# Kernel tuning notes

Measured on AMD Instinct MI355X. Metric: run time of the kernel, lower is better.

Reference implementation:

```python
import jax, jax.numpy as jnp
import numpy as np

R = 32
LORA_ALPHA = 64
SCALING = LORA_ALPHA / R  # 2.0
TOPK = 2
NOISE_EPS = 0.01


def setup_inputs() -> dict:
    key = jax.random.key(0)
    ks = jax.random.split(key, 7)
    B, S, D, OUT, E = 4, 2048, 4096, 4096, 8
    x = jax.random.normal(ks[0], (B, S, D), dtype=jnp.float32)
    eof_index = jax.random.randint(ks[1], (B,), 0, S)
    noise = jax.random.normal(ks[2], (B, E), dtype=jnp.float32)
    # learned params (random instead of the zero-init in reset_parameters so the
    # output is non-trivial); Linear weight layout is [out_features, in_features]
    A_w = jax.random.normal(ks[3], (R, D), dtype=jnp.float32) * (1.0 / np.sqrt(D))
    B_w = jax.random.normal(ks[4], (E, OUT, R), dtype=jnp.float32) * (1.0 / np.sqrt(R))
    route_w = jax.random.normal(ks[5], (E, D), dtype=jnp.float32) * (1.0 / np.sqrt(D))
    noise_w = jax.random.normal(ks[6], (E, D), dtype=jnp.float32) * (1.0 / np.sqrt(D))
    return {"x": x, "eof_index": eof_index, "noise": noise,
            "A_w": A_w, "B_w": B_w, "route_w": route_w, "noise_w": noise_w}


def reference(x, eof_index, noise, A_w, B_w, route_w, noise_w):
    B = x.shape[0]
    rows = jnp.arange(B)
    # routing input: token at eof_index for each batch row -> [B, D]
    routing_input = x[rows, eof_index]
    # noisy top-k gating (training path: noisy_gating and is_train are True)
    clean_logits = routing_input @ route_w.T                       # [B, E]
    noise_stddev = jax.nn.softplus(routing_input @ noise_w.T) + NOISE_EPS
    logits = clean_logits + noise * noise_stddev                   # [B, E]
    # torch code takes topk+1 then slices to topk; equivalent to top_k(topk)
    top_vals, top_idx = jax.lax.top_k(logits, TOPK)                # [B, K]
    top_gates = jax.nn.softmax(top_vals.astype(jnp.float32), axis=-1).astype(x.dtype)
    gates = jnp.zeros_like(logits).at[rows[:, None], top_idx].set(top_gates)  # [B, E]
    # shared low-rank projection
    shared = jnp.einsum('bsd,rd->bsr', x, A_w)                     # [B, S, r]
    # sum_i gate_i * (shared @ B_i^T), fused as one contraction
    lora_output = jnp.einsum('bsr,eor,be->bso', shared, B_w, gates)  # [B, S, out]
    return lora_output * SCALING
```

## Files before the change

### kernel.cpp

```cpp
#include <hip/hip_runtime.h>
#include <stdint.h>
#include <math.h>

#define B_ 4
#define S_ 2048
#define D_ 4096
#define O_ 4096
#define E_ 8
#define R_ 32
#define SCALING 2.0f
#define NOISE_EPS 0.01f

typedef unsigned short u16;
typedef short s16x8 __attribute__((ext_vector_type(8)));
typedef float f32x4 __attribute__((ext_vector_type(4)));

__device__ __forceinline__ float b2f(u16 u) {
  union { unsigned int i; float f; } v; v.i = ((unsigned int)u) << 16; return v.f;
}
__device__ __forceinline__ u16 f2b(float f) {
  union { unsigned int i; float f; } v; v.f = f;
  unsigned int i = v.i;
  return (u16)((i + 0x7FFFu + ((i >> 16) & 1u)) >> 16);
}
__device__ __forceinline__ void split2(float f, u16* h, u16* l) {
  u16 hi = f2b(f);
  *h = hi;
  *l = f2b(f - b2f(hi));
}

__device__ __forceinline__ float ld(const void* p, size_t i, int bf) {
  return bf ? b2f(((const u16*)p)[i]) : ((const float*)p)[i];
}

__global__ void k_detect(const unsigned int* __restrict__ xw, int* __restrict__ flag) {
  __shared__ int cnt;
  if (threadIdx.x == 0) cnt = 0;
  __syncthreads();
  unsigned int w = xw[threadIdx.x];
  unsigned int e = (w >> 7) & 0xFFu;
  if (e >= 90u && e <= 140u) atomicAdd(&cnt, 1);
  __syncthreads();
  if (threadIdx.x == 0) *flag = (cnt > 48) ? 1 : 0;
}

__global__ __launch_bounds__(256) void k_logits(
    const void* __restrict__ x, const int* __restrict__ eof,
    const void* __restrict__ route_w, const void* __restrict__ noise_w,
    const int* __restrict__ flag, float* __restrict__ wsf) {
  int bf = *flag;
  int be = blockIdx.x;
  int b = be >> 3, e = be & 7;
  size_t xoff = ((size_t)b * S_ + (size_t)eof[b]) * D_;
  size_t woff = (size_t)e * D_;
  float ac = 0.f, an = 0.f;
  for (int d = threadIdx.x; d < D_; d += 256) {
    float xv = ld(x, xoff + d, bf);
    ac += xv * ld(route_w, woff + d, bf);
    an += xv * ld(noise_w, woff + d, bf);
  }
  __shared__ float rc[256], rn[256];
  rc[threadIdx.x] = ac; rn[threadIdx.x] = an;
  __syncthreads();
  for (int s = 128; s > 0; s >>= 1) {
    if (threadIdx.x < (unsigned)s) {
      rc[threadIdx.x] += rc[threadIdx.x + s];
      rn[threadIdx.x] += rn[threadIdx.x + s];
    }
    __syncthreads();
  }
  if (threadIdx.x == 0) { wsf[16 + be] = rc[0]; wsf[48 + be] = rn[0]; }
}

__global__ void k_gates(const void* __restrict__ noise, const int* __restrict__ flag,
                        float* __restrict__ wsf) {
  int bf = *flag;
  int b = threadIdx.x;
  if (b >= B_) return;
  float lg[E_];
  for (int e = 0; e < E_; e++) {
    float c = wsf[16 + b * 8 + e];
    float n = wsf[48 + b * 8 + e];
    float sp = (n > 20.f) ? n : log1pf(expf(n));
    lg[e] = c + ld(noise, b * 8 + e, bf) * (sp + NOISE_EPS);
  }
  int i1 = 0; float v1 = lg[0];
  for (int e = 1; e < E_; e++) if (lg[e] > v1) { v1 = lg[e]; i1 = e; }
  int i2 = -1; float v2 = -3.0e38f;
  for (int e = 0; e < E_; e++) if (e != i1 && lg[e] > v2) { v2 = lg[e]; i2 = e; }
  float t = expf(v2 - v1);
  float g1 = 1.f / (1.f + t);
  float g2 = t / (1.f + t);
  for (int e = 0; e < E_; e++) wsf[80 + b * 8 + e] = 0.f;
  wsf[80 + b * 8 + i1] = g1;
  wsf[80 + b * 8 + i2] = g2;
}

__global__ __launch_bounds__(256) void k_prep(
    const void* __restrict__ Bw, const float* __restrict__ Aw,
    const int* __restrict__ flag, const float* __restrict__ gates,
    u16* __restrict__ Wph, u16* __restrict__ Wpl,
    u16* __restrict__ Aph, u16* __restrict__ Apl) {
  int bf = *flag;
  int blk = blockIdx.x;
  if (blk < 512) {
    int idx = blk * 256 + threadIdx.x;
    int b = idx >> 15;
    int u = idx & 32767;
    int o = u >> 3, rq = u & 7;
    float g[E_];
#pragma unroll
    for (int e = 0; e < E_; e++) g[e] = gates[b * 8 + e];
    f32x4 acc = {0.f, 0.f, 0.f, 0.f};
    if (bf) {
#pragma unroll
      for (int e = 0; e < E_; e++) {
        ushort4 v = ((const ushort4*)Bw)[(size_t)e * 32768 + u];
        acc[0] += g[e] * b2f(v.x);
        acc[1] += g[e] * b2f(v.y);
        acc[2] += g[e] * b2f(v.z);
        acc[3] += g[e] * b2f(v.w);
      }
    } else {
#pragma unroll
      for (int e = 0; e < E_; e++) {
        f32x4 v = ((const f32x4*)Bw)[(size_t)e * 32768 + u];
        acc += g[e] * v;
      }
    }
    acc *= SCALING;
    ushort4 h, l;
    split2(acc[0], &h.x, &l.x); split2(acc[1], &h.y, &l.y);
    split2(acc[2], &h.z, &l.z); split2(acc[3], &h.w, &l.w);
    int ot = o >> 4;
    int lane = ((rq >> 1) * 16) + (o & 15);
    size_t base = (((size_t)b * 256 + ot) * 64 + lane) * 8 + (rq & 1) * 4;
    *(ushort4*)(Wph + base) = h;
    *(ushort4*)(Wpl + base) = l;
  } else {
    if (bf) return;
    int flat = (blk - 512) * 256 + threadIdx.x;
    int k32idx = flat >> 7;
    int rem = flat & 127;
    int hf = rem >> 6;
    int lane = rem & 63;
    int r = hf * 16 + (lane & 15);
    int d = k32idx * 32 + (lane >> 4) * 8;
    const float* src = Aw + (size_t)r * D_ + d;
    f32x4 v0 = *(const f32x4*)src;
    f32x4 v1 = *(const f32x4*)(src + 4);
    ushort4 h0, l0, h1, l1;
    split2(v0[0], &h0.x, &l0.x); split2(v0[1], &h0.y, &l0.y);
    split2(v0[2], &h0.z, &l0.z); split2(v0[3], &h0.w, &l0.w);
    split2(v1[0], &h1.x, &l1.x); split2(v1[1], &h1.y, &l1.y);
    split2(v1[2], &h1.z, &l1.z); split2(v1[3], &h1.w, &l1.w);
    *(ushort4*)(Aph + (size_t)flat * 8)     = h0;
    *(ushort4*)(Aph + (size_t)flat * 8 + 4) = h1;
    *(ushort4*)(Apl + (size_t)flat * 8)     = l0;
    *(ushort4*)(Apl + (size_t)flat * 8 + 4) = l1;
  }
}

#define OCH 512
__global__ __launch_bounds__(256) void k_mega(
    const void* __restrict__ xv, const void* __restrict__ Awv,
    const u16* __restrict__ Aph, const u16* __restrict__ Apl,
    const u16* __restrict__ Wph, const u16* __restrict__ Wpl,
    const int* __restrict__ flag, void* __restrict__ out) {
  __shared__ union SM {
    struct { u16 xh[4096]; u16 xl[4096]; float red[4][512]; } p1;
    float C[16][516];
  } sm;
  __shared__ u16 shAh[512], shAl[512];
  int bf = *flag;
  int t = threadIdx.x;
  int lane = t & 63;
  int wave = t >> 6;
  int m = lane & 15, kg = lane >> 4;
  int row0 = blockIdx.x * 16;
  int b = row0 >> 11;

  f32x4 acc0 = {0.f, 0.f, 0.f, 0.f};
  f32x4 acc1 = {0.f, 0.f, 0.f, 0.f};
  if (bf) {
    int kbase = wave * 1024 + kg * 8;
    const u16* xp = (const u16*)xv + (size_t)(row0 + m) * D_ + kbase;
    const u16* a0 = (const u16*)Awv + (size_t)m * D_ + kbase;
    const u16* a1 = (const u16*)Awv + (size_t)(m + 16) * D_ + kbase;
#pragma unroll 4
    for (int k0 = 0; k0 < 1024; k0 += 32) {
      s16x8 a  = *(const s16x8*)(xp + k0);
      s16x8 b0 = *(const s16x8*)(a0 + k0);
      s16x8 b1 = *(const s16x8*)(a1 + k0);
      acc0 = __builtin_amdgcn_mfma_f32_16x16x32_bf16(a, b0, acc0, 0, 0, 0);
      acc1 = __builtin_amdgcn_mfma_f32_16x16x32_bf16(a, b1, acc1, 0, 0, 0);
    }
  } else {
    int srow = t >> 4;
    int sq = t & 15;
    const float* xrow = (const float*)xv + (size_t)(row0 + srow) * D_;
    for (int kc = 0; kc < D_; kc += 256) {
      __syncthreads();
#pragma unroll
      for (int q = 0; q < 4; q++) {
        int colf = (sq + q * 16) * 4;
        f32x4 v = *(const f32x4*)(xrow + kc + colf);
        ushort4 h, l;
        split2(v[0], &h.x, &l.x); split2(v[1], &h.y, &l.y);
        split2(v[2], &h.z, &l.z); split2(v[3], &h.w, &l.w);
        int swz = (srow * 512 + colf * 2) ^ ((srow & 7) << 4);
        *(ushort4*)((char*)sm.p1.xh + swz) = h;
        *(ushort4*)((char*)sm.p1.xl + swz) = l;
      }
      __syncthreads();
#pragma unroll
      for (int p = 0; p < 2; p++) {
        int k32 = (wave * 2 + p) * 32;
        int boff = (m * 512 + (k32 + kg * 8) * 2) ^ ((m & 7) << 4);
        s16x8 ah = *(const s16x8*)((const char*)sm.p1.xh + boff);
        s16x8 al = *(const s16x8*)((const char*)sm.p1.xl + boff);
        size_t k32idx = (size_t)(kc >> 5) + wave * 2 + p;
        const u16* ph = Aph + (k32idx * 2) * 512;
        const u16* pl = Apl + (k32idx * 2) * 512;
        s16x8 bh0 = *(const s16x8*)(ph + (size_t)lane * 8);
        s16x8 bl0 = *(const s16x8*)(pl + (size_t)lane * 8);
        s16x8 bh1 = *(const s16x8*)(ph + 512 + (size_t)lane * 8);
        s16x8 bl1 = *(const s16x8*)(pl + 512 + (size_t)lane * 8);
        acc0 = __builtin_amdgcn_mfma_f32_16x16x32_bf16(ah, bh0, acc0, 0, 0, 0);
        acc0 = __builtin_amdgcn_mfma_f32_16x16x32_bf16(ah, bl0, acc0, 0, 0, 0);
        acc0 = __builtin_amdgcn_mfma_f32_16x16x32_bf16(al, bh0, acc0, 0, 0, 0);
        acc1 = __builtin_amdgcn_mfma_f32_16x16x32_bf16(ah, bh1, acc1, 0, 0, 0);
        acc1 = __builtin_amdgcn_mfma_f32_16x16x32_bf16(ah, bl1, acc1, 0, 0, 0);
        acc1 = __builtin_amdgcn_mfma_f32_16x16x32_bf16(al, bh1, acc1, 0, 0, 0);
      }
    }
  }
  __syncthreads();
  int crow = (lane >> 4) * 4, ccol = lane & 15;
#pragma unroll
  for (int j = 0; j < 4; j++) {
    sm.p1.red[wave][(crow + j) * 32 + ccol]      = acc0[j];
    sm.p1.red[wave][(crow + j) * 32 + ccol + 16] = acc1[j];
  }
  __syncthreads();
#pragma unroll
  for (int q = 0; q < 2; q++) {
    int e = t + q * 256;
    float s = sm.p1.red[0][e] + sm.p1.red[1][e] + sm.p1.red[2][e] + sm.p1.red[3][e];
    u16 h, l;
    split2(s, &h, &l);
    int row = e >> 5, r = e & 31;
    int dst = ((r >> 3) * 16 + row) * 8 + (r & 7);
    shAh[dst] = h;
    shAl[dst] = l;
  }
  __syncthreads();

  s16x8 Ah = *(const s16x8*)(shAh + (size_t)lane * 8);
  s16x8 Al = *(const s16x8*)(shAl + (size_t)lane * 8);
  const u16* whB = Wph + (size_t)b * 131072;
  const u16* wlB = Wpl + (size_t)b * 131072;
  for (int oc = 0; oc < O_; oc += OCH) {
    __syncthreads();
#pragma unroll
    for (int i = 0; i < 8; i++) {
      int otc = wave * 8 + i;
      size_t otg = (size_t)((oc >> 4) + otc);
      s16x8 Bh = *(const s16x8*)(whB + otg * 512 + (size_t)lane * 8);
      s16x8 Bl = *(const s16x8*)(wlB + otg * 512 + (size_t)lane * 8);
      f32x4 acc = {0.f, 0.f, 0.f, 0.f};
      acc = __builtin_amdgcn_mfma_f32_16x16x32_bf16(Ah, Bh, acc, 0, 0, 0);
      acc = __builtin_amdgcn_mfma_f32_16x16x32_bf16(Ah, Bl, acc, 0, 0, 0);
      acc = __builtin_amdgcn_mfma_f32_16x16x32_bf16(Al, Bh, acc, 0, 0, 0);
      int ocol = otc * 16 + m;
#pragma unroll
      for (int j = 0; j < 4; j++) sm.C[crow + j][ocol] = acc[j];
    }
    __syncthreads();
#pragma unroll
    for (int it = 0; it < 8; it++) {
      int row = it * 2 + (t >> 7);
      int col = (t & 127) * 4;
      f32x4 v = *(const f32x4*)&sm.C[row][col];
      size_t off = (size_t)(row0 + row) * O_ + oc + col;
      if (bf) {
        ushort4 o4;
        o4.x = f2b(v[0]); o4.y = f2b(v[1]); o4.z = f2b(v[2]); o4.w = f2b(v[3]);
        *(ushort4*)((u16*)out + off) = o4;
      } else {
        *(f32x4*)((float*)out + off) = v;
      }
    }
  }
}

extern "C" void kernel_launch(void* const* d_in, const int* in_sizes, int n_in,
                              void* d_out, int out_size, void* d_ws, size_t ws_size,
                              hipStream_t stream) {
  const void* x       = d_in[0];
  const int*  eof     = (const int*)d_in[1];
  const void* noise   = d_in[2];
  const void* Aw      = d_in[3];
  const void* Bw      = d_in[4];
  const void* route_w = d_in[5];
  const void* noise_w = d_in[6];
  float* wsf = (float*)d_ws;
  int* flag = (int*)wsf;
  float* gates = wsf + 80;
  u16* Wph  = (u16*)(wsf + 112);
  u16* Wpl  = Wph + (size_t)B_ * O_ * R_;
  u16* Aph  = Wpl + (size_t)B_ * O_ * R_;
  u16* Apl  = Aph + (size_t)R_ * D_;

  k_detect<<<1, 64, 0, stream>>>((const unsigned int*)x, flag);
  k_logits<<<B_ * E_, 256, 0, stream>>>(x, eof, route_w, noise_w, flag, wsf);
  k_gates<<<1, 64, 0, stream>>>(noise, flag, wsf);
  k_prep<<<512 + 64, 256, 0, stream>>>(Bw, (const float*)Aw, flag, gates,
                                       Wph, Wpl, Aph, Apl);
  k_mega<<<(B_ * S_) / 16, 256, 0, stream>>>(x, Aw, Aph, Apl, Wph, Wpl,
                                             flag, d_out);
}
```

Measured before the change: 303.6 us.

## Split fused kernel into K-split projection and output-split expansion kernels

Removes the separate detect and gates kernels: each kernel now detects the input dtype with a wave ballot, and the gate computation is folded into k_prep. The single fused kernel is split in two. k_sharedP splits the D reduction four ways and writes partial rank-32 projections to a workspace buffer. k_outP sums those partials and computes a quarter of the output columns per block. This raises the block count from 512 to 2048 per stage for better CU occupancy and cuts launches, at the cost of an extra global round trip for the partials and redundant gate math per thread.

Result: faster. 285.8 us (median of 2 runs) (-5.8%).

```diff
diff --git a/kernel.cpp b/kernel.cpp
--- a/kernel.cpp
+++ b/kernel.cpp
@@ -33,22 +33,18 @@
   return bf ? b2f(((const u16*)p)[i]) : ((const float*)p)[i];
 }
 
-__global__ void k_detect(const unsigned int* __restrict__ xw, int* __restrict__ flag) {
-  __shared__ int cnt;
-  if (threadIdx.x == 0) cnt = 0;
-  __syncthreads();
-  unsigned int w = xw[threadIdx.x];
+__device__ __forceinline__ int detect_bf(const unsigned int* __restrict__ xw) {
+  unsigned int w = xw[threadIdx.x & 63];
   unsigned int e = (w >> 7) & 0xFFu;
-  if (e >= 90u && e <= 140u) atomicAdd(&cnt, 1);
-  __syncthreads();
-  if (threadIdx.x == 0) *flag = (cnt > 48) ? 1 : 0;
+  unsigned long long mask = __ballot((e >= 90u) && (e <= 140u));
+  return (__popcll(mask) > 48) ? 1 : 0;
 }
 
 __global__ __launch_bounds__(256) void k_logits(
     const void* __restrict__ x, const int* __restrict__ eof,
     const void* __restrict__ route_w, const void* __restrict__ noise_w,
-    const int* __restrict__ flag, float* __restrict__ wsf) {
-  int bf = *flag;
+    float* __restrict__ wsf) {
+  int bf = detect_bf((const unsigned int*)x);
   int be = blockIdx.x;
   int b = be >> 3, e = be & 7;
   size_t xoff = ((size_t)b * S_ + (size_t)eof[b]) * D_;
@@ -72,45 +68,40 @@
   if (threadIdx.x == 0) { wsf[16 + be] = rc[0]; wsf[48 + be] = rn[0]; }
 }
 
-__global__ void k_gates(const void* __restrict__ noise, const int* __restrict__ flag,
-                        float* __restrict__ wsf) {
-  int bf = *flag;
-  int b = threadIdx.x;
-  if (b >= B_) return;
-  float lg[E_];
-  for (int e = 0; e < E_; e++) {
-    float c = wsf[16 + b * 8 + e];
-    float n = wsf[48 + b * 8 + e];
-    float sp = (n > 20.f) ? n : log1pf(expf(n));
-    lg[e] = c + ld(noise, b * 8 + e, bf) * (sp + NOISE_EPS);
-  }
-  int i1 = 0; float v1 = lg[0];
-  for (int e = 1; e < E_; e++) if (lg[e] > v1) { v1 = lg[e]; i1 = e; }
-  int i2 = -1; float v2 = -3.0e38f;
-  for (int e = 0; e < E_; e++) if (e != i1 && lg[e] > v2) { v2 = lg[e]; i2 = e; }
-  float t = expf(v2 - v1);
-  float g1 = 1.f / (1.f + t);
-  float g2 = t / (1.f + t);
-  for (int e = 0; e < E_; e++) wsf[80 + b * 8 + e] = 0.f;
-  wsf[80 + b * 8 + i1] = g1;
-  wsf[80 + b * 8 + i2] = g2;
-}
-
 __global__ __launch_bounds__(256) void k_prep(
     const void* __restrict__ Bw, const float* __restrict__ Aw,
-    const int* __restrict__ flag, const float* __restrict__ gates,
+    const void* __restrict__ noise, const void* __restrict__ x,
+    const float* __restrict__ wsf,
     u16* __restrict__ Wph, u16* __restrict__ Wpl,
     u16* __restrict__ Aph, u16* __restrict__ Apl) {
-  int bf = *flag;
+  int bf = detect_bf((const unsigned int*)x);
   int blk = blockIdx.x;
   if (blk < 512) {
     int idx = blk * 256 + threadIdx.x;
     int b = idx >> 15;
+    float lg[E_];
+#pragma unroll
+    for (int e = 0; e < E_; e++) {
+      float c = wsf[16 + b * 8 + e];
+      float n = wsf[48 + b * 8 + e];
+      float sp = (n > 20.f) ? n : log1pf(expf(n));
+      lg[e] = c + ld(noise, b * 8 + e, bf) * (sp + NOISE_EPS);
+    }
+    int i1 = 0; float v1 = lg[0];
+#pragma unroll
+    for (int e = 1; e < E_; e++) if (lg[e] > v1) { v1 = lg[e]; i1 = e; }
+    int i2 = -1; float v2 = -3.0e38f;
+#pragma unroll
+    for (int e = 0; e < E_; e++) if (e != i1 && lg[e] > v2) { v2 = lg[e]; i2 = e; }
+    float tt = expf(v2 - v1);
+    float g1 = 1.f / (1.f + tt);
+    float g2 = tt / (1.f + tt);
+    float g[E_];
+#pragma unroll
+    for (int e = 0; e < E_; e++) g[e] = 0.f;
+    g[i1] = g1; g[i2] = g2;
     int u = idx & 32767;
     int o = u >> 3, rq = u & 7;
-    float g[E_];
-#pragma unroll
-    for (int e = 0; e < E_; e++) g[e] = gates[b * 8 + e];
     f32x4 acc = {0.f, 0.f, 0.f, 0.f};
     if (bf) {
 #pragma unroll
@@ -161,34 +152,31 @@
   }
 }
 
-#define OCH 512
-__global__ __launch_bounds__(256) void k_mega(
+__global__ __launch_bounds__(256) void k_sharedP(
     const void* __restrict__ xv, const void* __restrict__ Awv,
     const u16* __restrict__ Aph, const u16* __restrict__ Apl,
-    const u16* __restrict__ Wph, const u16* __restrict__ Wpl,
-    const int* __restrict__ flag, void* __restrict__ out) {
-  __shared__ union SM {
-    struct { u16 xh[4096]; u16 xl[4096]; float red[4][512]; } p1;
-    float C[16][516];
+    float* __restrict__ pbuf) {
+  __shared__ union {
+    struct { u16 xh[4096]; u16 xl[4096]; } s;
+    float red4[4][512];
   } sm;
-  __shared__ u16 shAh[512], shAl[512];
-  int bf = *flag;
+  int bf = detect_bf((const unsigned int*)xv);
   int t = threadIdx.x;
   int lane = t & 63;
   int wave = t >> 6;
   int m = lane & 15, kg = lane >> 4;
-  int row0 = blockIdx.x * 16;
-  int b = row0 >> 11;
-
+  int rowgrp = blockIdx.x >> 2;
+  int dq = blockIdx.x & 3;
+  int row0 = rowgrp * 16;
   f32x4 acc0 = {0.f, 0.f, 0.f, 0.f};
   f32x4 acc1 = {0.f, 0.f, 0.f, 0.f};
   if (bf) {
-    int kbase = wave * 1024 + kg * 8;
+    int kbase = dq * 1024 + wave * 256 + kg * 8;
     const u16* xp = (const u16*)xv + (size_t)(row0 + m) * D_ + kbase;
     const u16* a0 = (const u16*)Awv + (size_t)m * D_ + kbase;
     const u16* a1 = (const u16*)Awv + (size_t)(m + 16) * D_ + kbase;
-#pragma unroll 4
-    for (int k0 = 0; k0 < 1024; k0 += 32) {
+#pragma unroll
+    for (int k0 = 0; k0 < 256; k0 += 32) {
       s16x8 a  = *(const s16x8*)(xp + k0);
       s16x8 b0 = *(const s16x8*)(a0 + k0);
       s16x8 b1 = *(const s16x8*)(a1 + k0);
@@ -198,30 +186,30 @@
   } else {
     int srow = t >> 4;
     int sq = t & 15;
-    const float* xrow = (const float*)xv + (size_t)(row0 + srow) * D_;
-    for (int kc = 0; kc < D_; kc += 256) {
+    const float* xrow = (const float*)xv + (size_t)(row0 + srow) * D_ + dq * 1024;
+    for (int c = 0; c < 4; c++) {
       __syncthreads();
 #pragma unroll
       for (int q = 0; q < 4; q++) {
         int colf = (sq + q * 16) * 4;
-        f32x4 v = *(const f32x4*)(xrow + kc + colf);
+        f32x4 v = *(const f32x4*)(xrow + c * 256 + colf);
         ushort4 h, l;
         split2(v[0], &h.x, &l.x); split2(v[1], &h.y, &l.y);
         split2(v[2], &h.z, &l.z); split2(v[3], &h.w, &l.w);
         int swz = (srow * 512 + colf * 2) ^ ((srow & 7) << 4);
-        *(ushort4*)((char*)sm.p1.xh + swz) = h;
-        *(ushort4*)((char*)sm.p1.xl + swz) = l;
+        *(ushort4*)((char*)sm.s.xh + swz) = h;
+        *(ushort4*)((char*)sm.s.xl + swz) = l;
       }
       __syncthreads();
 #pragma unroll
-      for (int p = 0; p < 2; p++) {
-        int k32 = (wave * 2 + p) * 32;
+      for (int p2 = 0; p2 < 2; p2++) {
+        int k32 = (wave * 2 + p2) * 32;
         int boff = (m * 512 + (k32 + kg * 8) * 2) ^ ((m & 7) << 4);
-        s16x8 ah = *(const s16x8*)((const char*)sm.p1.xh + boff);
-        s16x8 al = *(const s16x8*)((const char*)sm.p1.xl + boff);
-        size_t k32idx = (size_t)(kc >> 5) + wave * 2 + p;
-        const u16* ph = Aph + (k32idx * 2) * 512;
-        const u16* pl = Apl + (k32idx * 2) * 512;
+        s16x8 ah = *(const s16x8*)((const char*)sm.s.xh + boff);
+        s16x8 al = *(const s16x8*)((const char*)sm.s.xl + boff);
+        int k32idx = dq * 32 + c * 8 + wave * 2 + p2;
+        const u16* ph = Aph + (size_t)k32idx * 1024;
+        const u16* pl = Apl + (size_t)k32idx * 1024;
         s16x8 bh0 = *(const s16x8*)(ph + (size_t)lane * 8);
         s16x8 bl0 = *(const s16x8*)(pl + (size_t)lane * 8);
         s16x8 bh1 = *(const s16x8*)(ph + 512 + (size_t)lane * 8);
@@ -239,33 +227,66 @@
   int crow = (lane >> 4) * 4, ccol = lane & 15;
 #pragma unroll
   for (int j = 0; j < 4; j++) {
-    sm.p1.red[wave][(crow + j) * 32 + ccol]      = acc0[j];
-    sm.p1.red[wave][(crow + j) * 32 + ccol + 16] = acc1[j];
+    sm.red4[wave][(crow + j) * 32 + ccol]      = acc0[j];
+    sm.red4[wave][(crow + j) * 32 + ccol + 16] = acc1[j];
   }
   __syncthreads();
-#pragma unroll
-  for (int q = 0; q < 2; q++) {
-    int e = t + q * 256;
-    float s = sm.p1.red[0][e] + sm.p1.red[1][e] + sm.p1.red[2][e] + sm.p1.red[3][e];
+  if (t < 64) {
+    int row = t & 15, rq = t >> 4;
+    f32x4 va, vb;
+#pragma unroll
+    for (int j = 0; j < 4; j++) {
+      int e = row * 32 + rq * 8 + j;
+      va[j] = sm.red4[0][e] + sm.red4[1][e] + sm.red4[2][e] + sm.red4[3][e];
+    }
+#pragma unroll
+    for (int j = 0; j < 4; j++) {
+      int e = row * 32 + rq * 8 + 4 + j;
+      vb[j] = sm.red4[0][e] + sm.red4[1][e] + sm.red4[2][e] + sm.red4[3][e];
+    }
+    float* pp = pbuf + ((size_t)rowgrp * 4 + dq) * 512 + t * 8;
+    *(f32x4*)pp = va;
+    *(f32x4*)(pp + 4) = vb;
+  }
+}
+
+__global__ __launch_bounds__(256) void k_outP(
+    const void* __restrict__ xv, const float* __restrict__ pbuf,
+    const u16* __restrict__ Wph, const u16* __restrict__ Wpl,
+    void* __restrict__ out) {
+  __shared__ float C[16][260];
+  int bf = detect_bf((const unsigned int*)xv);
+  int t = threadIdx.x;
+  int lane = t & 63, wave = t >> 6, m = lane & 15;
+  int rowgrp = blockIdx.x >> 2;
+  int oq = blockIdx.x & 3;
+  int row0 = rowgrp * 16;
+  int b = row0 >> 11;
+  const float* pp = pbuf + (size_t)rowgrp * 4 * 512;
+  f32x4 sa = {0.f, 0.f, 0.f, 0.f}, sb = {0.f, 0.f, 0.f, 0.f};
+#pragma unroll
+  for (int dq = 0; dq < 4; dq++) {
+    sa += *(const f32x4*)(pp + dq * 512 + (size_t)lane * 8);
+    sb += *(const f32x4*)(pp + dq * 512 + (size_t)lane * 8 + 4);
+  }
+  s16x8 Ah, Al;
+  {
     u16 h, l;
-    split2(s, &h, &l);
-    int row = e >> 5, r = e & 31;
-    int dst = ((r >> 3) * 16 + row) * 8 + (r & 7);
-    shAh[dst] = h;
-    shAl[dst] = l;
-  }
-  __syncthreads();
-
-  s16x8 Ah = *(const s16x8*)(shAh + (size_t)lane * 8);
-  s16x8 Al = *(const s16x8*)(shAl + (size_t)lane * 8);
+#pragma unroll
+    for (int j = 0; j < 4; j++) {
+      split2(sa[j], &h, &l); Ah[j] = (short)h; Al[j] = (short)l;
+      split2(sb[j], &h, &l); Ah[4 + j] = (short)h; Al[4 + j] = (short)l;
+    }
+  }
+  int crow = (lane >> 4) * 4;
   const u16* whB = Wph + (size_t)b * 131072;
   const u16* wlB = Wpl + (size_t)b * 131072;
-  for (int oc = 0; oc < O_; oc += OCH) {
-    __syncthreads();
-#pragma unroll
-    for (int i = 0; i < 8; i++) {
-      int otc = wave * 8 + i;
-      size_t otg = (size_t)((oc >> 4) + otc);
+  for (int cc = 0; cc < 4; cc++) {
+    int tbase = oq * 64 + cc * 16;
+#pragma unroll
+    for (int i = 0; i < 4; i++) {
+      int otc = wave * 4 + i;
+      size_t otg = (size_t)(tbase + otc);
       s16x8 Bh = *(const s16x8*)(whB + otg * 512 + (size_t)lane * 8);
       s16x8 Bl = *(const s16x8*)(wlB + otg * 512 + (size_t)lane * 8);
       f32x4 acc = {0.f, 0.f, 0.f, 0.f};
@@ -274,15 +295,15 @@
       acc = __builtin_amdgcn_mfma_f32_16x16x32_bf16(Al, Bh, acc, 0, 0, 0);
       int ocol = otc * 16 + m;
 #pragma unroll
-      for (int j = 0; j < 4; j++) sm.C[crow + j][ocol] = acc[j];
+      for (int j = 0; j < 4; j++) C[crow + j][ocol] = acc[j];
     }
     __syncthreads();
 #pragma unroll
-    for (int it = 0; it < 8; it++) {
-      int row = it * 2 + (t >> 7);
-      int col = (t & 127) * 4;
-      f32x4 v = *(const f32x4*)&sm.C[row][col];
-      size_t off = (size_t)(row0 + row) * O_ + oc + col;
+    for (int pass = 0; pass < 4; pass++) {
+      int row = pass * 4 + (t >> 6);
+      int col = (t & 63) * 4;
+      f32x4 v = *(const f32x4*)&C[row][col];
+      size_t off = (size_t)(row0 + row) * O_ + oq * 1024 + cc * 256 + col;
       if (bf) {
         ushort4 o4;
         o4.x = f2b(v[0]); o4.y = f2b(v[1]); o4.z = f2b(v[2]); o4.w = f2b(v[3]);
@@ -291,6 +312,7 @@
         *(f32x4*)((float*)out + off) = v;
       }
     }
+    __syncthreads();
   }
 }
 
@@ -305,18 +327,15 @@
   const void* route_w = d_in[5];
   const void* noise_w = d_in[6];
   float* wsf = (float*)d_ws;
-  int* flag = (int*)wsf;
-  float* gates = wsf + 80;
   u16* Wph  = (u16*)(wsf + 112);
   u16* Wpl  = Wph + (size_t)B_ * O_ * R_;
   u16* Aph  = Wpl + (size_t)B_ * O_ * R_;
   u16* Apl  = Aph + (size_t)R_ * D_;
-
-  k_detect<<<1, 64, 0, stream>>>((const unsigned int*)x, flag);
-  k_logits<<<B_ * E_, 256, 0, stream>>>(x, eof, route_w, noise_w, flag, wsf);
-  k_gates<<<1, 64, 0, stream>>>(noise, flag, wsf);
-  k_prep<<<512 + 64, 256, 0, stream>>>(Bw, (const float*)Aw, flag, gates,
+  float* pbuf = (float*)(Apl + (size_t)R_ * D_);
+
+  k_logits<<<B_ * E_, 256, 0, stream>>>(x, eof, route_w, noise_w, wsf);
+  k_prep<<<512 + 64, 256, 0, stream>>>(Bw, (const float*)Aw, noise, x, wsf,
                                        Wph, Wpl, Aph, Apl);
-  k_mega<<<(B_ * S_) / 16, 256, 0, stream>>>(x, Aw, Aph, Apl, Wph, Wpl,
-                                             flag, d_out);
-}
+  k_sharedP<<<2048, 256, 0, stream>>>(x, Aw, Aph, Apl, pbuf);
+  k_outP<<<2048, 256, 0, stream>>>(x, pbuf, Wph, Wpl, d_out);
+}
```
